# Optimization experiments

Measured on AMD Instinct MI355X. Metric: run time of the kernel, lower is better.

The kernel has to match this reference:

```python
import jax, jax.numpy as jnp
import numpy as np

B, H, N, D = 8, 12, 2048, 64
M = 256  # DCT truncation length (maxM)
HEAD_DIM = D


def create_dct(n, m):
    # Orthonormal DCT-II basis, truncated to first m frequencies: [m, n]
    k = jnp.arange(m, dtype=jnp.float32)[:, None]
    i = jnp.arange(n, dtype=jnp.float32)[None, :]
    Dm = jnp.cos(jnp.pi * (2.0 * i + 1.0) * k / (2.0 * n)) * jnp.sqrt(2.0 / n)
    Dm = Dm.at[0].multiply(1.0 / jnp.sqrt(2.0))
    return Dm


def setup_inputs() -> dict:
    key = jax.random.key(0)
    kq, kk, kv = jax.random.split(key, 3)
    Q = jax.random.normal(kq, (B, H, N, D), dtype=jnp.float32)
    K = jax.random.normal(kk, (B, H, N, D), dtype=jnp.float32)
    V = jax.random.normal(kv, (B, H, N, D), dtype=jnp.float32)
    mask = jnp.ones((B, N), dtype=jnp.float32)
    Q_dct = create_dct(N, M)
    return {"Q": Q, "K": K, "V": V, "mask": mask, "Q_dct": Q_dct}


def reference(Q, K, V, mask, Q_dct):
    scale = 1.0 / jnp.sqrt(jnp.sqrt(jnp.float32(HEAD_DIM)))
    m4 = mask[:, None, :, None]  # [B,1,N,1]
    Qs = Q * scale
    Ks = K * scale * m4
    Vs = V * m4
    # DCT projection along the sequence axis: [m,n] x [b,h,n,d] -> [b,h,m,d]
    Qd = jnp.einsum('mn,bhnd->bhmd', Q_dct, Qs)
    Kd = jnp.einsum('mn,bhnd->bhmd', Q_dct, Ks)
    Vd = jnp.einsum('mn,bhnd->bhmd', Q_dct, Vs)
    energy = jnp.einsum('bhmd,bhkd->bhmk', Qd, Kd)  # [B,H,M,M]
    attention = jax.nn.softmax(energy, axis=-1)
    ctx = jnp.einsum('bhmk,bhkd->bhmd', attention, Vd)
    # inverse DCT reconstruction: Q_dct^T @ ctx -> [B,H,N,D]
    x = jnp.einsum('mn,bhmd->bhnd', Q_dct, ctx)
    return x
```

## Files before the change

### kernel.cpp

```cpp
#include <hip/hip_runtime.h>
#include <hip/hip_bf16.h>
#include <cstddef>

#define B_ 8
#define H_ 12
#define N_ 2048
#define D_ 64
#define M_ 256
#define BH_ (B_*H_)

typedef __attribute__((ext_vector_type(8))) short short8v;
typedef __attribute__((ext_vector_type(4))) float f32x4;

static __device__ __forceinline__ float4 ld4(const float* p){ return *(const float4*)p; }

static __device__ __forceinline__ unsigned short f2bf(float x){
    union { float f; unsigned int u; } v; v.f = x;
    unsigned int r = v.u + 0x7FFFu + ((v.u >> 16) & 1u);
    return (unsigned short)(r >> 16);
}
static __device__ __forceinline__ unsigned int pack2(float a, float b){
    return (unsigned int)f2bf(a) | ((unsigned int)f2bf(b) << 16);
}

__global__ __launch_bounds__(256)
void dct_prep_kernel(const float* __restrict__ Dct, unsigned short* __restrict__ DctA,
                     unsigned short* __restrict__ DctT)
{
    __shared__ __align__(16) unsigned short T[64*72];
    const int n0 = blockIdx.x * 64, m0 = blockIdx.y * 64;
    const int tid = threadIdx.x;
    const int mrow = tid >> 2, ng = tid & 3;
    const int m = m0 + mrow;
    unsigned short h[16];
    #pragma unroll
    for (int j = 0; j < 4; ++j) {
        const float4 t = ld4(Dct + (size_t)m*N_ + n0 + ng*16 + j*4);
        h[4*j+0]=f2bf(t.x); h[4*j+1]=f2bf(t.y); h[4*j+2]=f2bf(t.z); h[4*j+3]=f2bf(t.w);
    }
    unsigned int w[8];
    #pragma unroll
    for (int j = 0; j < 8; ++j) w[j] = (unsigned int)h[2*j] | ((unsigned int)h[2*j+1]<<16);
    const int fm = m >> 4;
    #pragma unroll
    for (int s = 0; s < 2; ++s) {
        const int u = 2*ng + s;
        const int fk = (n0 >> 5) + (u >> 2);
        const int lane = (m & 15) + (u & 3) * 16;
        unsigned short* dst = DctA + ((size_t)(fm*64 + fk)*64 + lane)*8;
        *(uint4*)dst = *(uint4*)&w[s*4];
    }
    #pragma unroll
    for (int j = 0; j < 16; ++j) T[(ng*16+j)*72 + mrow] = h[j];
    __syncthreads();
    const int n = tid >> 2, mg = tid & 3;
    uint4 a  = *(uint4*)&T[n*72 + mg*16];
    uint4 b2 = *(uint4*)&T[n*72 + mg*16 + 8];
    unsigned short* dt = DctT + (size_t)(n0+n)*M_ + m0 + mg*16;
    *(uint4*)dt = a; *(uint4*)(dt+8) = b2;
}

__global__ __launch_bounds__(256, 2)
void gemm_qkv(const float* __restrict__ Q, const float* __restrict__ K,
              const float* __restrict__ V, const float* __restrict__ mask,
              const unsigned short* __restrict__ DctA,
              float* __restrict__ Qd, float* __restrict__ Kd, float* __restrict__ Vd)
{
    __shared__ __align__(16) unsigned short Bsw[2][64*128];
    __shared__ __align__(16) float Msk[N_];
    const int wg = blockIdx.x;
    const int id = (wg & 7) * 72 + (wg >> 3);
    const int half  = id & 1;
    const int panel = id >> 1;
    const int bh = panel % BH_;
    const int tz = panel / BH_;
    const int b  = bh / H_;
    const float scale = 0.35355339059327373f;
    const float* X; float* Y; float smul; int um;
    if (tz==0)      { X=Q; Y=Qd; smul=scale; um=0; }
    else if (tz==1) { X=K; Y=Kd; smul=scale; um=1; }
    else            { X=V; Y=Vd; smul=1.0f;  um=1; }
    X += (size_t)bh*N_*D_;
    Y += (size_t)bh*M_*D_ + (size_t)half*128*D_;

    const int tid  = threadIdx.x;
    const int lane = tid & 63, wv = tid >> 6;
    const unsigned short* abase = DctA + (size_t)(half*8 + wv*2)*32768 + (size_t)lane*8;
    const float* xcol = X + lane;
    const int swz = (lane & 7) << 4;

    f32x4 acc[2][4];
    #pragma unroll
    for (int i = 0; i < 2; ++i)
        #pragma unroll
        for (int j = 0; j < 4; ++j) { acc[i][j].x=0.f; acc[i][j].y=0.f; acc[i][j].z=0.f; acc[i][j].w=0.f; }

    short8v pa[2][4], pb[2][4];
    float xrA[32], xrB[32];

    #define A_LOAD(P, T) do {                                                 \
        _Pragma("unroll")                                                     \
        for (int mf_ = 0; mf_ < 2; ++mf_)                                     \
            _Pragma("unroll")                                                 \
            for (int kh_ = 0; kh_ < 4; ++kh_)                                 \
                P[mf_][kh_] = *(const short8v*)(abase + (size_t)(mf_*64 + 4*(T)+kh_)*512); \
    } while(0)

    #define X_LOAD(XR, K0) do {                                               \
        const float* xp_ = xcol + (size_t)((K0) + wv*32) * D_;                \
        _Pragma("unroll")                                                     \
        for (int i_ = 0; i_ < 32; ++i_) XR[i_] = xp_[(size_t)i_*D_];          \
    } while(0)

    #define WRITE_B(XR, BUF, K0) do {                                         \
        const float4* mrow_ = (const float4*)&Msk[(K0) + wv*32];              \
        float fmv_[32];                                                       \
        _Pragma("unroll")                                                     \
        for (int j_ = 0; j_ < 8; ++j_) {                                      \
            const float4 t_ = mrow_[j_];                                      \
            fmv_[4*j_]=t_.x; fmv_[4*j_+1]=t_.y; fmv_[4*j_+2]=t_.z; fmv_[4*j_+3]=t_.w; \
        }                                                                     \
        _Pragma("unroll")                                                     \
        for (int c_ = 0; c_ < 4; ++c_) {                                      \
            uint4 w_;                                                         \
            w_.x = pack2(XR[8*c_+0]*fmv_[8*c_+0], XR[8*c_+1]*fmv_[8*c_+1]);   \
            w_.y = pack2(XR[8*c_+2]*fmv_[8*c_+2], XR[8*c_+3]*fmv_[8*c_+3]);   \
            w_.z = pack2(XR[8*c_+4]*fmv_[8*c_+4], XR[8*c_+5]*fmv_[8*c_+5]);   \
            w_.w = pack2(XR[8*c_+6]*fmv_[8*c_+6], XR[8*c_+7]*fmv_[8*c_+7]);   \
            *(uint4*)((char*)&Bsw[BUF][0] + lane*256 + ((wv*64 + c_*16) ^ swz)) = w_; \
        }                                                                     \
    } while(0)

    #define COMPUTE(BUF, P) do {                                              \
        _Pragma("unroll")                                                     \
        for (int kh_ = 0; kh_ < 4; ++kh_) {                                   \
            const int colb_ = kh_*64 + (lane>>4)*16;                          \
            short8v b_[4];                                                    \
            _Pragma("unroll")                                                 \
            for (int nf_ = 0; nf_ < 4; ++nf_) {                               \
                const int rr_ = nf_*16 + (lane&15);                           \
                b_[nf_] = *(const short8v*)((char*)&Bsw[BUF][0] + rr_*256 + (colb_ ^ ((rr_&7)<<4))); \
            }                                                                 \
            _Pragma("unroll")                                                 \
            for (int mf_ = 0; mf_ < 2; ++mf_)                                 \
                _Pragma("unroll")                                             \
                for (int nf_ = 0; nf_ < 4; ++nf_)                             \
                    acc[mf_][nf_] = __builtin_amdgcn_mfma_f32_16x16x32_bf16(P[mf_][kh_], b_[nf_], acc[mf_][nf_], 0, 0, 0); \
        }                                                                     \
    } while(0)

    #define BARJ() do { asm volatile("s_waitcnt lgkmcnt(0)" ::: "memory");    \
                        __builtin_amdgcn_sched_barrier(0);                    \
                        __builtin_amdgcn_s_barrier(); } while(0)

    {
        #pragma unroll
        for (int c = 0; c < 2; ++c) {
            const int idx = (tid + c*256) * 4;
            float4 v;
            if (um) {
                v = ld4(mask + (size_t)b*N_ + idx);
                v.x *= smul; v.y *= smul; v.z *= smul; v.w *= smul;
            } else { v.x = smul; v.y = smul; v.z = smul; v.w = smul; }
            *(float4*)&Msk[idx] = v;
        }
    }
    A_LOAD(pa, 0);
    X_LOAD(xrA, 0);
    X_LOAD(xrB, 128);
    __syncthreads();
    WRITE_B(xrA, 0, 0);
    BARJ();

    #define STEP_EVEN(T) do {                                                 \
        A_LOAD(pb, (T)+1);                                                    \
        X_LOAD(xrA, ((T)+2)*128);                                             \
        COMPUTE(0, pa);                                                       \
        __builtin_amdgcn_sched_barrier(0);                                    \
        WRITE_B(xrB, 1, ((T)+1)*128);                                         \
        BARJ();                                                               \
    } while(0)
    #define STEP_ODD(T) do {                                                  \
        A_LOAD(pa, (T)+1);                                                    \
        X_LOAD(xrB, ((T)+2)*128);                                             \
        COMPUTE(1, pb);                                                       \
        __builtin_amdgcn_sched_barrier(0);                                    \
        WRITE_B(xrA, 0, ((T)+1)*128);                                         \
        BARJ();                                                               \
    } while(0)

    for (int tb = 0; tb < 14; tb += 2) {
        STEP_EVEN(tb);
        STEP_ODD(tb+1);
    }
    A_LOAD(pb, 15);
    COMPUTE(0, pa);
    __builtin_amdgcn_sched_barrier(0);
    WRITE_B(xrB, 1, 15*128);
    BARJ();
    COMPUTE(1, pb);

    #pragma unroll
    for (int mf = 0; mf < 2; ++mf)
        #pragma unroll
        for (int nf = 0; nf < 4; ++nf)
            #pragma unroll
            for (int r = 0; r < 4; ++r) {
                const int m = wv*32 + mf*16 + (lane>>4)*4 + r;
                const int d = nf*16 + (lane&15);
                Y[(size_t)m*D_ + d] = acc[mf][nf][r];
            }
    #undef A_LOAD
    #undef X_LOAD
    #undef WRITE_B
    #undef COMPUTE
    #undef BARJ
    #undef STEP_EVEN
    #undef STEP_ODD
}

__global__ __launch_bounds__(256, 2)
void attn_kernel(const float* __restrict__ Qd, const float* __restrict__ Kd,
                 const float* __restrict__ Vd, unsigned short* __restrict__ CtxT)
{
    __shared__ __align__(16) char LB[65536];
    unsigned short* QA = (unsigned short*)(LB);
    unsigned short* KB = (unsigned short*)(LB + 8192);
    unsigned short* PL = (unsigned short*)(LB);
    unsigned short* VT = (unsigned short*)(LB + 32768);
    unsigned short* T  = (unsigned short*)(LB);

    const int mt = blockIdx.x, bh = blockIdx.y;
    const float* qd = Qd + (size_t)bh*M_*D_ + (size_t)mt*64*D_;
    const float* kd = Kd + (size_t)bh*M_*D_;
    const float* vd = Vd + (size_t)bh*M_*D_;
    const int tid  = threadIdx.x;
    const int lane = tid & 63, wv = tid >> 6;
    const int l15  = lane & 15, kg = lane >> 4;
    const int swz  = (l15 & 7) << 4;

    {
        const int row = tid >> 2, q = tid & 3;
        {
            const float* p = qd + (size_t)row*D_ + q*16;
            const float4 a = ld4(p), b2 = ld4(p+4), c = ld4(p+8), d = ld4(p+12);
            uint4 w0, w1;
            w0.x=pack2(a.x,a.y);  w0.y=pack2(a.z,a.w);  w0.z=pack2(b2.x,b2.y); w0.w=pack2(b2.z,b2.w);
            w1.x=pack2(c.x,c.y);  w1.y=pack2(c.z,c.w);  w1.z=pack2(d.x,d.y);  w1.w=pack2(d.z,d.w);
            const int s = (row & 7) << 4;
            *(uint4*)((char*)QA + row*128 + ((q*32)      ^ s)) = w0;
            *(uint4*)((char*)QA + row*128 + ((q*32 + 16) ^ s)) = w1;
        }
        #pragma unroll
        for (int c0 = 0; c0 < 4; ++c0) {
            const int krow = c0*64 + row;
            const float* p = kd + (size_t)krow*D_ + q*16;
            const float4 a = ld4(p), b2 = ld4(p+4), c = ld4(p+8), d = ld4(p+12);
            uint4 w0, w1;
            w0.x=pack2(a.x,a.y);  w0.y=pack2(a.z,a.w);  w0.z=pack2(b2.x,b2.y); w0.w=pack2(b2.z,b2.w);
            w1.x=pack2(c.x,c.y);  w1.y=pack2(c.z,c.w);  w1.z=pack2(d.x,d.y);  w1.w=pack2(d.z,d.w);
            const int s = (krow & 7) << 4;
            *(uint4*)((char*)KB + krow*128 + ((q*32)      ^ s)) = w0;
            *(uint4*)((char*)KB + krow*128 + ((q*32 + 16) ^ s)) = w1;
        }
    }
    __syncthreads();

    f32x4 acc[16];
    #pragma unroll
    for (int i = 0; i < 16; ++i) { acc[i].x=0.f; acc[i].y=0.f; acc[i].z=0.f; acc[i].w=0.f; }
    #pragma unroll
    for (int kh = 0; kh < 2; ++kh) {
        const int colb = kh*64 + kg*16;
        const short8v af = *(const short8v*)((char*)QA + (wv*16 + l15)*128 + (colb ^ swz));
        #pragma unroll
        for (int nf = 0; nf < 16; ++nf) {
            const short8v bf = *(const short8v*)((char*)KB + (nf*16 + l15)*128 + (colb ^ swz));
            acc[nf] = __builtin_amdgcn_mfma_f32_16x16x32_bf16(af, bf, acc[nf], 0, 0, 0);
        }
    }

    float inv[4];
    #pragma unroll
    for (int r = 0; r < 4; ++r) {
        float mx = acc[0][r];
        #pragma unroll
        for (int nf = 1; nf < 16; ++nf) mx = fmaxf(mx, acc[nf][r]);
        mx = fmaxf(mx, __shfl_xor(mx, 1));
        mx = fmaxf(mx, __shfl_xor(mx, 2));
        mx = fmaxf(mx, __shfl_xor(mx, 4));
        mx = fmaxf(mx, __shfl_xor(mx, 8));
        float sm = 0.f;
        #pragma unroll
        for (int nf = 0; nf < 16; ++nf) {
            const float p = __expf(acc[nf][r] - mx);
            acc[nf][r] = p; sm += p;
        }
        sm += __shfl_xor(sm, 1);
        sm += __shfl_xor(sm, 2);
        sm += __shfl_xor(sm, 4);
        sm += __shfl_xor(sm, 8);
        inv[r] = 1.0f / sm;
    }
    __syncthreads();

    {
        const int rowbase = wv*16 + kg*4;
        #pragma unroll
        for (int nf = 0; nf < 16; ++nf)
            #pragma unroll
            for (int r = 0; r < 4; ++r) {
                const int rowP = rowbase + r;
                const int byte = rowP*512 + ((((nf*16 + l15)*2)) ^ ((rowP & 7) << 4));
                *(unsigned short*)((char*)PL + byte) = f2bf(acc[nf][r]);
            }
    }
    {
        const int dcol = tid & 63, kq = tid >> 6;
        const int vs = (dcol & 7) << 4;
        #pragma unroll
        for (int cp = 0; cp < 32; ++cp) {
            const int k2 = kq*64 + cp*2;
            const float v0 = vd[(size_t)k2*D_ + dcol];
            const float v1 = vd[(size_t)(k2+1)*D_ + dcol];
            const int byte = dcol*512 + ((k2*2) ^ vs);
            *(unsigned int*)((char*)VT + byte) = pack2(v0, v1);
        }
    }
    __syncthreads();

    f32x4 c2[4];
    #pragma unroll
    for (int i = 0; i < 4; ++i) { c2[i].x=0.f; c2[i].y=0.f; c2[i].z=0.f; c2[i].w=0.f; }
    #pragma unroll
    for (int kf = 0; kf < 8; ++kf) {
        const int colb = kf*64 + kg*16;
        const short8v a = *(const short8v*)((char*)PL + (wv*16 + l15)*512 + (colb ^ swz));
        #pragma unroll
        for (int nf2 = 0; nf2 < 4; ++nf2) {
            const int drow = nf2*16 + l15;
            const short8v bb = *(const short8v*)((char*)VT + drow*512 + (colb ^ swz));
            c2[nf2] = __builtin_amdgcn_mfma_f32_16x16x32_bf16(a, bb, c2[nf2], 0, 0, 0);
        }
    }
    __syncthreads();

    {
        const int rowbase = wv*16 + kg*4;
        #pragma unroll
        for (int nf2 = 0; nf2 < 4; ++nf2)
            #pragma unroll
            for (int r = 0; r < 4; ++r) {
                const int d = nf2*16 + l15;
                T[d*72 + rowbase + r] = f2bf(c2[nf2][r] * inv[r]);
            }
    }
    __syncthreads();
    {
        const int d2 = tid >> 2, mg = tid & 3;
        uint4 w0 = *(uint4*)&T[d2*72 + mg*16];
        uint4 w1 = *(uint4*)&T[d2*72 + mg*16 + 8];
        unsigned short* dst = CtxT + (size_t)bh*D_*M_ + (size_t)d2*M_ + mt*64 + mg*16;
        *(uint4*)dst = w0; *(uint4*)(dst+8) = w1;
    }
}

__global__ __launch_bounds__(128, 2)
void gemm_out(const unsigned short* __restrict__ DctT, const unsigned short* __restrict__ CtxT,
              float* __restrict__ Out)
{
    __shared__ __align__(16) unsigned short Asw[128*64];
    __shared__ __align__(16) unsigned short Bsw[64*64];
    const int nt = blockIdx.x, bh = blockIdx.y;
    const int n0 = nt*128;
    const unsigned short* ct = CtxT + (size_t)bh*D_*M_;
    float* out = Out + (size_t)bh*N_*D_;
    const int tid = threadIdx.x;
    const int lane = tid & 63, wave = tid >> 6;

    f32x4 acc[4][4];
    #pragma unroll
    for (int i = 0; i < 4; ++i)
        #pragma unroll
        for (int j = 0; j < 4; ++j) { acc[i][j].x=0.f; acc[i][j].y=0.f; acc[i][j].z=0.f; acc[i][j].w=0.f; }

    for (int step = 0; step < 4; ++step) {
        const int k0 = step*64;
        if (step) __syncthreads();
        const int ch = tid & 7;
        #pragma unroll
        for (int rr = 0; rr < 8; ++rr) {
            const int r = (tid>>3) + rr*16;
            const uint4 v = *(const uint4*)(DctT + (size_t)(n0+r)*M_ + k0 + ch*8);
            *(uint4*)((char*)Asw + r*128 + ((ch*16) ^ ((r&7)<<4))) = v;
        }
        #pragma unroll
        for (int rr = 0; rr < 4; ++rr) {
            const int d = (tid>>3) + rr*16;
            const uint4 v = *(const uint4*)(ct + (size_t)d*M_ + k0 + ch*8);
            *(uint4*)((char*)Bsw + d*128 + ((ch*16) ^ (((d>>1)&7)<<4))) = v;
        }
        __syncthreads();
        #pragma unroll
        for (int kh = 0; kh < 2; ++kh) {
            const int colb = kh*64 + (lane>>4)*16;
            short8v a[4], bb[4];
            #pragma unroll
            for (int mf = 0; mf < 4; ++mf) {
                const int r = wave*64 + mf*16 + (lane&15);
                a[mf] = *(const short8v*)((char*)Asw + r*128 + (colb ^ ((r&7)<<4)));
            }
            #pragma unroll
            for (int nf = 0; nf < 4; ++nf) {
                const int r = nf*16 + (lane&15);
                bb[nf] = *(const short8v*)((char*)Bsw + r*128 + (colb ^ (((r>>1)&7)<<4)));
            }
            #pragma unroll
            for (int mf = 0; mf < 4; ++mf)
                #pragma unroll
                for (int nf = 0; nf < 4; ++nf)
                    acc[mf][nf] = __builtin_amdgcn_mfma_f32_16x16x32_bf16(a[mf], bb[nf], acc[mf][nf], 0, 0, 0);
        }
    }
    #pragma unroll
    for (int mf = 0; mf < 4; ++mf)
        #pragma unroll
        for (int nf = 0; nf < 4; ++nf)
            #pragma unroll
            for (int r = 0; r < 4; ++r) {
                const int n = n0 + wave*64 + mf*16 + (lane>>4)*4 + r;
                const int d = nf*16 + (lane&15);
                out[(size_t)n*D_ + d] = acc[mf][nf][r];
            }
}

extern "C" void kernel_launch(void* const* d_in, const int* in_sizes, int n_in,
                              void* d_out, int out_size, void* d_ws, size_t ws_size,
                              hipStream_t stream) {
    const float* Q    = (const float*)d_in[0];
    const float* K    = (const float*)d_in[1];
    const float* V    = (const float*)d_in[2];
    const float* mask = (const float*)d_in[3];
    const float* Dct  = (const float*)d_in[4];
    float* out = (float*)d_out;

    const size_t per = (size_t)BH_ * M_ * D_;
    float* wsf = (float*)d_ws;
    float* Qd = wsf;
    float* Kd = Qd + per;
    float* Vd = Kd + per;
    unsigned short* CtxT = (unsigned short*)(Vd + per);
    unsigned short* DctA = CtxT + per;
    unsigned short* DctT = DctA + (size_t)M_ * N_;

    dct_prep_kernel<<<dim3(N_/64, M_/64), 256, 0, stream>>>(Dct, DctA, DctT);
    gemm_qkv<<<dim3(576), 256, 0, stream>>>(Q, K, V, mask, DctA, Qd, Kd, Vd);
    attn_kernel<<<dim3(M_/64, BH_), 256, 0, stream>>>(Qd, Kd, Vd, CtxT);
    gemm_out<<<dim3(N_/128, BH_), 128, 0, stream>>>(DctT, CtxT, out);
}
```

Measured before the change: 84.56 us.

## Split QKV DCT projection into four 64-row M tiles per panel

The QKV projection GEMM now splits each (tensor, bh) panel into four 64-row output tiles instead of two 128-row halves. This doubles the grid to 1152 workgroups, halves per-wave accumulator and A-fragment registers, and raises the launch-bounds occupancy hint to 4. The aim is better occupancy and latency hiding across the 256 CUs. The cost is that each X panel (Q/K/V slice) is now read from global memory and converted to bf16 in LDS four times instead of twice, doubling that input traffic and conversion work.

```diff
diff --git a/kernel.cpp b/kernel.cpp
--- a/kernel.cpp
+++ b/kernel.cpp
@@ -60,7 +60,7 @@
     *(uint4*)dt = a; *(uint4*)(dt+8) = b2;
 }
 
-__global__ __launch_bounds__(256, 2)
+__global__ __launch_bounds__(256, 4)
 void gemm_qkv(const float* __restrict__ Q, const float* __restrict__ K,
               const float* __restrict__ V, const float* __restrict__ mask,
               const unsigned short* __restrict__ DctA,
@@ -69,9 +69,9 @@
     __shared__ __align__(16) unsigned short Bsw[2][64*128];
     __shared__ __align__(16) float Msk[N_];
     const int wg = blockIdx.x;
-    const int id = (wg & 7) * 72 + (wg >> 3);
-    const int half  = id & 1;
-    const int panel = id >> 1;
+    const int id = (wg & 7) * 144 + (wg >> 3);
+    const int mt    = id & 3;
+    const int panel = id >> 2;
     const int bh = panel % BH_;
     const int tz = panel / BH_;
     const int b  = bh / H_;
@@ -81,29 +81,25 @@
     else if (tz==1) { X=K; Y=Kd; smul=scale; um=1; }
     else            { X=V; Y=Vd; smul=1.0f;  um=1; }
     X += (size_t)bh*N_*D_;
-    Y += (size_t)bh*M_*D_ + (size_t)half*128*D_;
+    Y += (size_t)bh*M_*D_ + (size_t)mt*64*D_;
 
     const int tid  = threadIdx.x;
     const int lane = tid & 63, wv = tid >> 6;
-    const unsigned short* abase = DctA + (size_t)(half*8 + wv*2)*32768 + (size_t)lane*8;
+    const unsigned short* abase = DctA + (size_t)(mt*4 + wv)*32768 + (size_t)lane*8;
     const float* xcol = X + lane;
     const int swz = (lane & 7) << 4;
 
-    f32x4 acc[2][4];
-    #pragma unroll
-    for (int i = 0; i < 2; ++i)
-        #pragma unroll
-        for (int j = 0; j < 4; ++j) { acc[i][j].x=0.f; acc[i][j].y=0.f; acc[i][j].z=0.f; acc[i][j].w=0.f; }
-
-    short8v pa[2][4], pb[2][4];
+    f32x4 acc[4];
+    #pragma unroll
+    for (int j = 0; j < 4; ++j) { acc[j].x=0.f; acc[j].y=0.f; acc[j].z=0.f; acc[j].w=0.f; }
+
+    short8v pa[4], pb[4];
     float xrA[32], xrB[32];
 
     #define A_LOAD(P, T) do {                                                 \
         _Pragma("unroll")                                                     \
-        for (int mf_ = 0; mf_ < 2; ++mf_)                                     \
-            _Pragma("unroll")                                                 \
-            for (int kh_ = 0; kh_ < 4; ++kh_)                                 \
-                P[mf_][kh_] = *(const short8v*)(abase + (size_t)(mf_*64 + 4*(T)+kh_)*512); \
+        for (int kh_ = 0; kh_ < 4; ++kh_)                                     \
+            P[kh_] = *(const short8v*)(abase + (size_t)(4*(T)+kh_)*512);      \
     } while(0)
 
     #define X_LOAD(XR, K0) do {                                               \
@@ -135,17 +131,12 @@
         _Pragma("unroll")                                                     \
         for (int kh_ = 0; kh_ < 4; ++kh_) {                                   \
             const int colb_ = kh_*64 + (lane>>4)*16;                          \
-            short8v b_[4];                                                    \
             _Pragma("unroll")                                                 \
             for (int nf_ = 0; nf_ < 4; ++nf_) {                               \
                 const int rr_ = nf_*16 + (lane&15);                           \
-                b_[nf_] = *(const short8v*)((char*)&Bsw[BUF][0] + rr_*256 + (colb_ ^ ((rr_&7)<<4))); \
+                const short8v b_ = *(const short8v*)((char*)&Bsw[BUF][0] + rr_*256 + (colb_ ^ ((rr_&7)<<4))); \
+                acc[nf_] = __builtin_amdgcn_mfma_f32_16x16x32_bf16(P[kh_], b_, acc[nf_], 0, 0, 0); \
             }                                                                 \
-            _Pragma("unroll")                                                 \
-            for (int mf_ = 0; mf_ < 2; ++mf_)                                 \
-                _Pragma("unroll")                                             \
-                for (int nf_ = 0; nf_ < 4; ++nf_)                             \
-                    acc[mf_][nf_] = __builtin_amdgcn_mfma_f32_16x16x32_bf16(P[mf_][kh_], b_[nf_], acc[mf_][nf_], 0, 0, 0); \
         }                                                                     \
     } while(0)
 
@@ -201,15 +192,13 @@
     COMPUTE(1, pb);
 
     #pragma unroll
-    for (int mf = 0; mf < 2; ++mf)
-        #pragma unroll
-        for (int nf = 0; nf < 4; ++nf)
-            #pragma unroll
-            for (int r = 0; r < 4; ++r) {
-                const int m = wv*32 + mf*16 + (lane>>4)*4 + r;
-                const int d = nf*16 + (lane&15);
-                Y[(size_t)m*D_ + d] = acc[mf][nf][r];
-            }
+    for (int nf = 0; nf < 4; ++nf)
+        #pragma unroll
+        for (int r = 0; r < 4; ++r) {
+            const int m = wv*16 + (lane>>4)*4 + r;
+            const int d = nf*16 + (lane&15);
+            Y[(size_t)m*D_ + d] = acc[nf][r];
+        }
     #undef A_LOAD
     #undef X_LOAD
     #undef WRITE_B
@@ -454,7 +443,7 @@
     unsigned short* DctT = DctA + (size_t)M_ * N_;
 
     dct_prep_kernel<<<dim3(N_/64, M_/64), 256, 0, stream>>>(Dct, DctA, DctT);
-    gemm_qkv<<<dim3(576), 256, 0, stream>>>(Q, K, V, mask, DctA, Qd, Kd, Vd);
+    gemm_qkv<<<dim3(1152), 256, 0, stream>>>(Q, K, V, mask, DctA, Qd, Kd, Vd);
     attn_kernel<<<dim3(M_/64, BH_), 256, 0, stream>>>(Qd, Kd, Vd, CtxT);
     gemm_out<<<dim3(N_/128, BH_), 128, 0, stream>>>(DctT, CtxT, out);
 }
```

Result: slower. 90.17 us (+6.6%).

## Split QKV DCT projection along sequence into two partial sums reduced in attention

Applied to the files above, without the earlier changes.

Adds a split-K variant of the QKV projection GEMM. Each block uses 512 threads with 8 waves, covers the full M=256 output, and handles half of the N=2048 reduction. It writes two partial results to workspace, and the attention kernel sums them while loading Q/K/V. This gives each block a shorter serial reduction and more waves per block, at the cost of extra workspace writes and reads for the partials. The compute loop also interleaves the B-fragment loads with the MFMAs to reduce register pressure. The old path remains as a fallback when the workspace is too small.

```diff
diff --git a/kernel.cpp b/kernel.cpp
--- a/kernel.cpp
+++ b/kernel.cpp
@@ -60,11 +60,166 @@
     *(uint4*)dt = a; *(uint4*)(dt+8) = b2;
 }
 
+__global__ __launch_bounds__(512, 4)
+void gemm_qkv_ks(const float* __restrict__ Q, const float* __restrict__ K,
+                 const float* __restrict__ V, const float* __restrict__ mask,
+                 const unsigned short* __restrict__ DctA, float* __restrict__ Part)
+{
+    __shared__ __align__(16) unsigned short Bsw[2][64*128];
+    __shared__ __align__(16) float Msk[1024];
+    const size_t per = (size_t)BH_ * M_ * D_;
+    const int wg = blockIdx.x;
+    const int id = (wg & 7) * 72 + (wg >> 3);
+    const int kh    = id & 1;
+    const int panel = id >> 1;
+    const int bh = panel % BH_;
+    const int tz = panel / BH_;
+    const int b  = bh / H_;
+    const float scale = 0.35355339059327373f;
+    const float* X; float smul; int um;
+    if (tz==0)      { X=Q; smul=scale; um=0; }
+    else if (tz==1) { X=K; smul=scale; um=1; }
+    else            { X=V; smul=1.0f;  um=1; }
+    X += (size_t)bh*N_*D_ + (size_t)kh*1024*D_;
+    float* Y = Part + ((size_t)tz*2 + kh)*per + (size_t)bh*M_*D_;
+
+    const int tid  = threadIdx.x;
+    const int lane = tid & 63, wv = tid >> 6;
+    const unsigned short* abase = DctA + (size_t)(wv*2)*32768 + (size_t)lane*8;
+    const int fkb = kh*32;
+    const float* xcol = X + (tid & 63);
+    const int dd  = tid & 63;
+    const int swz = (dd & 7) << 4;
+
+    f32x4 acc[2][4];
+    #pragma unroll
+    for (int i = 0; i < 2; ++i)
+        #pragma unroll
+        for (int j = 0; j < 4; ++j) { acc[i][j].x=0.f; acc[i][j].y=0.f; acc[i][j].z=0.f; acc[i][j].w=0.f; }
+
+    short8v pa[2][4], pb[2][4];
+    float xrA[16], xrB[16];
+
+    #define A_LOAD(P, T) do {                                                 \
+        _Pragma("unroll")                                                     \
+        for (int mf_ = 0; mf_ < 2; ++mf_)                                     \
+            _Pragma("unroll")                                                 \
+            for (int j_ = 0; j_ < 4; ++j_)                                    \
+                P[mf_][j_] = *(const short8v*)(abase + (size_t)(mf_*64 + fkb + 4*(T)+j_)*512); \
+    } while(0)
+
+    #define X_LOAD(XR, T) do {                                                \
+        const float* xp_ = xcol + (size_t)((T)*128 + wv*16) * D_;             \
+        _Pragma("unroll")                                                     \
+        for (int i_ = 0; i_ < 16; ++i_) XR[i_] = xp_[(size_t)i_*D_];          \
+    } while(0)
+
+    #define WRITE_B(XR, BUF, T) do {                                          \
+        const float4* mrow_ = (const float4*)&Msk[(T)*128 + wv*16];           \
+        float fmv_[16];                                                       \
+        _Pragma("unroll")                                                     \
+        for (int j_ = 0; j_ < 4; ++j_) {                                      \
+            const float4 t_ = mrow_[j_];                                      \
+            fmv_[4*j_]=t_.x; fmv_[4*j_+1]=t_.y; fmv_[4*j_+2]=t_.z; fmv_[4*j_+3]=t_.w; \
+        }                                                                     \
+        _Pragma("unroll")                                                     \
+        for (int c_ = 0; c_ < 2; ++c_) {                                      \
+            uint4 w_;                                                         \
+            w_.x = pack2(XR[8*c_+0]*fmv_[8*c_+0], XR[8*c_+1]*fmv_[8*c_+1]);   \
+            w_.y = pack2(XR[8*c_+2]*fmv_[8*c_+2], XR[8*c_+3]*fmv_[8*c_+3]);   \
+            w_.z = pack2(XR[8*c_+4]*fmv_[8*c_+4], XR[8*c_+5]*fmv_[8*c_+5]);   \
+            w_.w = pack2(XR[8*c_+6]*fmv_[8*c_+6], XR[8*c_+7]*fmv_[8*c_+7]);   \
+            *(uint4*)((char*)&Bsw[BUF][0] + dd*256 + ((wv*32 + c_*16) ^ swz)) = w_; \
+        }                                                                     \
+    } while(0)
+
+    #define COMPUTE(BUF, P) do {                                              \
+        _Pragma("unroll")                                                     \
+        for (int kh_ = 0; kh_ < 4; ++kh_) {                                   \
+            const int colb_ = kh_*64 + (lane>>4)*16;                          \
+            _Pragma("unroll")                                                 \
+            for (int nf_ = 0; nf_ < 4; ++nf_) {                               \
+                const int rr_ = nf_*16 + (lane&15);                           \
+                const short8v b_ = *(const short8v*)((char*)&Bsw[BUF][0] + rr_*256 + (colb_ ^ ((rr_&7)<<4))); \
+                _Pragma("unroll")                                             \
+                for (int mf_ = 0; mf_ < 2; ++mf_)                             \
+                    acc[mf_][nf_] = __builtin_amdgcn_mfma_f32_16x16x32_bf16(P[mf_][kh_], b_, acc[mf_][nf_], 0, 0, 0); \
+            }                                                                 \
+        }                                                                     \
+    } while(0)
+
+    #define BARJ() do { asm volatile("s_waitcnt lgkmcnt(0)" ::: "memory");    \
+                        __builtin_amdgcn_sched_barrier(0);                    \
+                        __builtin_amdgcn_s_barrier(); } while(0)
+
+    {
+        const int idx = tid * 2;
+        float2 v;
+        if (um) {
+            v = *(const float2*)(mask + (size_t)b*N_ + kh*1024 + idx);
+            v.x *= smul; v.y *= smul;
+        } else { v.x = smul; v.y = smul; }
+        *(float2*)&Msk[idx] = v;
+    }
+    A_LOAD(pa, 0);
+    X_LOAD(xrA, 0);
+    X_LOAD(xrB, 1);
+    __syncthreads();
+    WRITE_B(xrA, 0, 0);
+    BARJ();
+
+    #define STEP_EVEN(T) do {                                                 \
+        A_LOAD(pb, (T)+1);                                                    \
+        X_LOAD(xrA, (T)+2);                                                   \
+        COMPUTE(0, pa);                                                       \
+        __builtin_amdgcn_sched_barrier(0);                                    \
+        WRITE_B(xrB, 1, (T)+1);                                               \
+        BARJ();                                                               \
+    } while(0)
+    #define STEP_ODD(T) do {                                                  \
+        A_LOAD(pa, (T)+1);                                                    \
+        X_LOAD(xrB, (T)+2);                                                   \
+        COMPUTE(1, pb);                                                       \
+        __builtin_amdgcn_sched_barrier(0);                                    \
+        WRITE_B(xrA, 0, (T)+1);                                               \
+        BARJ();                                                               \
+    } while(0)
+
+    for (int tb = 0; tb < 6; tb += 2) {
+        STEP_EVEN(tb);
+        STEP_ODD(tb+1);
+    }
+    A_LOAD(pb, 7);
+    COMPUTE(0, pa);
+    __builtin_amdgcn_sched_barrier(0);
+    WRITE_B(xrB, 1, 7);
+    BARJ();
+    COMPUTE(1, pb);
+
+    #pragma unroll
+    for (int mf = 0; mf < 2; ++mf)
+        #pragma unroll
+        for (int nf = 0; nf < 4; ++nf)
+            #pragma unroll
+            for (int r = 0; r < 4; ++r) {
+                const int m = wv*32 + mf*16 + (lane>>4)*4 + r;
+                const int d = nf*16 + (lane&15);
+                Y[(size_t)m*D_ + d] = acc[mf][nf][r];
+            }
+    #undef A_LOAD
+    #undef X_LOAD
+    #undef WRITE_B
+    #undef COMPUTE
+    #undef BARJ
+    #undef STEP_EVEN
+    #undef STEP_ODD
+}
+
 __global__ __launch_bounds__(256, 2)
-void gemm_qkv(const float* __restrict__ Q, const float* __restrict__ K,
-              const float* __restrict__ V, const float* __restrict__ mask,
-              const unsigned short* __restrict__ DctA,
-              float* __restrict__ Qd, float* __restrict__ Kd, float* __restrict__ Vd)
+void gemm_qkv_full(const float* __restrict__ Q, const float* __restrict__ K,
+                   const float* __restrict__ V, const float* __restrict__ mask,
+                   const unsigned short* __restrict__ DctA,
+                   float* __restrict__ Qd, float* __restrict__ Kd, float* __restrict__ Vd)
 {
     __shared__ __align__(16) unsigned short Bsw[2][64*128];
     __shared__ __align__(16) float Msk[N_];
@@ -135,17 +290,14 @@
         _Pragma("unroll")                                                     \
         for (int kh_ = 0; kh_ < 4; ++kh_) {                                   \
             const int colb_ = kh_*64 + (lane>>4)*16;                          \
-            short8v b_[4];                                                    \
             _Pragma("unroll")                                                 \
             for (int nf_ = 0; nf_ < 4; ++nf_) {                               \
                 const int rr_ = nf_*16 + (lane&15);                           \
-                b_[nf_] = *(const short8v*)((char*)&Bsw[BUF][0] + rr_*256 + (colb_ ^ ((rr_&7)<<4))); \
+                const short8v b_ = *(const short8v*)((char*)&Bsw[BUF][0] + rr_*256 + (colb_ ^ ((rr_&7)<<4))); \
+                _Pragma("unroll")                                             \
+                for (int mf_ = 0; mf_ < 2; ++mf_)                             \
+                    acc[mf_][nf_] = __builtin_amdgcn_mfma_f32_16x16x32_bf16(P[mf_][kh_], b_, acc[mf_][nf_], 0, 0, 0); \
             }                                                                 \
-            _Pragma("unroll")                                                 \
-            for (int mf_ = 0; mf_ < 2; ++mf_)                                 \
-                _Pragma("unroll")                                             \
-                for (int nf_ = 0; nf_ < 4; ++nf_)                             \
-                    acc[mf_][nf_] = __builtin_amdgcn_mfma_f32_16x16x32_bf16(P[mf_][kh_], b_[nf_], acc[mf_][nf_], 0, 0, 0); \
         }                                                                     \
     } while(0)
 
@@ -220,8 +372,10 @@
 }
 
 __global__ __launch_bounds__(256, 2)
-void attn_kernel(const float* __restrict__ Qd, const float* __restrict__ Kd,
-                 const float* __restrict__ Vd, unsigned short* __restrict__ CtxT)
+void attn_kernel(const float* __restrict__ QdA, const float* __restrict__ QdB,
+                 const float* __restrict__ KdA, const float* __restrict__ KdB,
+                 const float* __restrict__ VdA, const float* __restrict__ VdB,
+                 unsigned short* __restrict__ CtxT, int dual)
 {
     __shared__ __align__(16) char LB[65536];
     unsigned short* QA = (unsigned short*)(LB);
@@ -231,9 +385,8 @@
     unsigned short* T  = (unsigned short*)(LB);
 
     const int mt = blockIdx.x, bh = blockIdx.y;
-    const float* qd = Qd + (size_t)bh*M_*D_ + (size_t)mt*64*D_;
-    const float* kd = Kd + (size_t)bh*M_*D_;
-    const float* vd = Vd + (size_t)bh*M_*D_;
+    const size_t qoff = (size_t)bh*M_*D_ + (size_t)mt*64*D_;
+    const size_t koff = (size_t)bh*M_*D_;
     const int tid  = threadIdx.x;
     const int lane = tid & 63, wv = tid >> 6;
     const int l15  = lane & 15, kg = lane >> 4;
@@ -242,8 +395,16 @@
     {
         const int row = tid >> 2, q = tid & 3;
         {
-            const float* p = qd + (size_t)row*D_ + q*16;
-            const float4 a = ld4(p), b2 = ld4(p+4), c = ld4(p+8), d = ld4(p+12);
+            const float* p = QdA + qoff + (size_t)row*D_ + q*16;
+            float4 a = ld4(p), b2 = ld4(p+4), c = ld4(p+8), d = ld4(p+12);
+            if (dual) {
+                const float* p2 = QdB + qoff + (size_t)row*D_ + q*16;
+                const float4 e=ld4(p2), f=ld4(p2+4), g=ld4(p2+8), h2=ld4(p2+12);
+                a.x+=e.x; a.y+=e.y; a.z+=e.z; a.w+=e.w;
+                b2.x+=f.x; b2.y+=f.y; b2.z+=f.z; b2.w+=f.w;
+                c.x+=g.x; c.y+=g.y; c.z+=g.z; c.w+=g.w;
+                d.x+=h2.x; d.y+=h2.y; d.z+=h2.z; d.w+=h2.w;
+            }
             uint4 w0, w1;
             w0.x=pack2(a.x,a.y);  w0.y=pack2(a.z,a.w);  w0.z=pack2(b2.x,b2.y); w0.w=pack2(b2.z,b2.w);
             w1.x=pack2(c.x,c.y);  w1.y=pack2(c.z,c.w);  w1.z=pack2(d.x,d.y);  w1.w=pack2(d.z,d.w);
@@ -254,8 +415,16 @@
         #pragma unroll
         for (int c0 = 0; c0 < 4; ++c0) {
             const int krow = c0*64 + row;
-            const float* p = kd + (size_t)krow*D_ + q*16;
-            const float4 a = ld4(p), b2 = ld4(p+4), c = ld4(p+8), d = ld4(p+12);
+            const float* p = KdA + koff + (size_t)krow*D_ + q*16;
+            float4 a = ld4(p), b2 = ld4(p+4), c = ld4(p+8), d = ld4(p+12);
+            if (dual) {
+                const float* p2 = KdB + koff + (size_t)krow*D_ + q*16;
+                const float4 e=ld4(p2), f=ld4(p2+4), g=ld4(p2+8), h2=ld4(p2+12);
+                a.x+=e.x; a.y+=e.y; a.z+=e.z; a.w+=e.w;
+                b2.x+=f.x; b2.y+=f.y; b2.z+=f.z; b2.w+=f.w;
+                c.x+=g.x; c.y+=g.y; c.z+=g.z; c.w+=g.w;
+                d.x+=h2.x; d.y+=h2.y; d.z+=h2.z; d.w+=h2.w;
+            }
             uint4 w0, w1;
             w0.x=pack2(a.x,a.y);  w0.y=pack2(a.z,a.w);  w0.z=pack2(b2.x,b2.y); w0.w=pack2(b2.z,b2.w);
             w1.x=pack2(c.x,c.y);  w1.y=pack2(c.z,c.w);  w1.z=pack2(d.x,d.y);  w1.w=pack2(d.z,d.w);
@@ -321,8 +490,12 @@
         #pragma unroll
         for (int cp = 0; cp < 32; ++cp) {
             const int k2 = kq*64 + cp*2;
-            const float v0 = vd[(size_t)k2*D_ + dcol];
-            const float v1 = vd[(size_t)(k2+1)*D_ + dcol];
+            float v0 = VdA[koff + (size_t)k2*D_ + dcol];
+            float v1 = VdA[koff + (size_t)(k2+1)*D_ + dcol];
+            if (dual) {
+                v0 += VdB[koff + (size_t)k2*D_ + dcol];
+                v1 += VdB[koff + (size_t)(k2+1)*D_ + dcol];
+            }
             const int byte = dcol*512 + ((k2*2) ^ vs);
             *(unsigned int*)((char*)VT + byte) = pack2(v0, v1);
         }
@@ -445,16 +618,35 @@
     float* out = (float*)d_out;
 
     const size_t per = (size_t)BH_ * M_ * D_;
-    float* wsf = (float*)d_ws;
-    float* Qd = wsf;
-    float* Kd = Qd + per;
-    float* Vd = Kd + per;
-    unsigned short* CtxT = (unsigned short*)(Vd + per);
-    unsigned short* DctA = CtxT + per;
-    unsigned short* DctT = DctA + (size_t)M_ * N_;
-
-    dct_prep_kernel<<<dim3(N_/64, M_/64), 256, 0, stream>>>(Dct, DctA, DctT);
-    gemm_qkv<<<dim3(576), 256, 0, stream>>>(Q, K, V, mask, DctA, Qd, Kd, Vd);
-    attn_kernel<<<dim3(M_/64, BH_), 256, 0, stream>>>(Qd, Kd, Vd, CtxT);
-    gemm_out<<<dim3(N_/128, BH_), 128, 0, stream>>>(DctT, CtxT, out);
-}
+    const size_t need_new = 6*per*sizeof(float) + per*sizeof(unsigned short)
+                          + 2*(size_t)M_*N_*sizeof(unsigned short);
+
+    if (ws_size >= need_new) {
+        float* Part = (float*)d_ws;
+        unsigned short* CtxT = (unsigned short*)(Part + 6*per);
+        unsigned short* DctA = CtxT + per;
+        unsigned short* DctT = DctA + (size_t)M_*N_;
+
+        dct_prep_kernel<<<dim3(N_/64, M_/64), 256, 0, stream>>>(Dct, DctA, DctT);
+        gemm_qkv_ks<<<dim3(576), 512, 0, stream>>>(Q, K, V, mask, DctA, Part);
+        attn_kernel<<<dim3(M_/64, BH_), 256, 0, stream>>>(
+            Part + 0*per, Part + 1*per,
+            Part + 2*per, Part + 3*per,
+            Part + 4*per, Part + 5*per,
+            CtxT, 1);
+        gemm_out<<<dim3(N_/128, BH_), 128, 0, stream>>>(DctT, CtxT, out);
+    } else {
+        float* wsf = (float*)d_ws;
+        float* Qd = wsf;
+        float* Kd = Qd + per;
+        float* Vd = Kd + per;
+        unsigned short* CtxT = (unsigned short*)(Vd + per);
+        unsigned short* DctA = CtxT + per;
+        unsigned short* DctT = DctA + (size_t)M_*N_;
+
+        dct_prep_kernel<<<dim3(N_/64, M_/64), 256, 0, stream>>>(Dct, DctA, DctT);
+        gemm_qkv_full<<<dim3(576), 256, 0, stream>>>(Q, K, V, mask, DctA, Qd, Kd, Vd);
+        attn_kernel<<<dim3(M_/64, BH_), 256, 0, stream>>>(Qd, Qd, Kd, Kd, Vd, Vd, CtxT, 0);
+        gemm_out<<<dim3(N_/128, BH_), 128, 0, stream>>>(DctT, CtxT, out);
+    }
+}
```

New measurement: 104.5 us. 23.6% more time.
